# Kernel tuning notes

Hardware: AMD Instinct MI355X
Metric: run time of the kernel (lower is better)

## Reference

```python
import jax, jax.numpy as jnp
import numpy as np
from jax import lax

B, C_IN, C_OUT, KK, KS = 8, 32, 64, 4, 3
D, H, W = 32, 64, 64
PAD = 1

def setup_inputs() -> dict:
    key = jax.random.key(0)
    ks = jax.random.split(key, 12)
    s = 0.02
    return {
        "x": jax.random.normal(ks[0], (B, C_IN, D, H, W), jnp.float32),
        # K candidate conv kernels and biases
        "weight": jax.random.normal(ks[1], (KK, C_OUT, C_IN, KS, KS, KS), jnp.float32) * s,
        "cbias": jnp.zeros((KK, C_OUT), jnp.float32),
        "temperature": jnp.float32(34.0),
        # attention key path: BN(affine, eval-mode) -> GELU -> 1x1 conv (linear)
        "bn1_g": jnp.ones((C_IN,), jnp.float32),
        "bn1_b": jnp.zeros((C_IN,), jnp.float32),
        "w1": jax.random.normal(ks[2], (C_IN, C_IN), jnp.float32) * s,
        "b1": jnp.zeros((C_IN,), jnp.float32),
        "bn2_g": jnp.ones((C_IN,), jnp.float32),
        "bn2_b": jnp.zeros((C_IN,), jnp.float32),
        "w2": jax.random.normal(ks[3], (C_IN, C_IN), jnp.float32) * s,
        "b2": jnp.zeros((C_IN,), jnp.float32),
        "bn3_g": jnp.ones((C_IN,), jnp.float32),
        "bn3_b": jnp.zeros((C_IN,), jnp.float32),
        "w3": jax.random.normal(ks[4], (KK, C_IN), jnp.float32) * s,
        "b3": jnp.zeros((KK,), jnp.float32),
    }

def _attention(p, temperature, bn1_g, bn1_b, w1, b1, bn2_g, bn2_b, w2, b2, bn3_g, bn3_b, w3, b3):
    # p: [B, C] pooled features. 1x1x1 convs on 1x1x1 maps == linear layers.
    gelu = lambda t: jax.nn.gelu(t, approximate=False)  # torch nn.GELU default is erf
    a = gelu(p * bn1_g + bn1_b)          # BN (eval: rm=0, rv=1) + GELU
    a = a @ w1.T + b1
    a = gelu(a * bn2_g + bn2_b)
    a = a @ w2.T + b2
    a = a + p                            # ResidualLayer (plain add)
    a = a * bn3_g + bn3_b
    logits = a @ w3.T + b3               # [B, K]
    return jax.nn.softmax(logits / temperature, axis=1)

def reference(x, weight, cbias, temperature, bn1_g, bn1_b, w1, b1,
              bn2_g, bn2_b, w2, b2, bn3_g, bn3_b, w3, b3):
    # x: [B, C_in, D, H, W]
    p = x.mean(axis=(2, 3, 4))  # AdaptiveAvgPool3d(1)
    attn = _attention(p, temperature, bn1_g, bn1_b, w1, b1,
                      bn2_g, bn2_b, w2, b2, bn3_g, bn3_b, w3, b3)  # [B, K]
    # per-sample aggregated kernels / bias
    agg_w = jnp.einsum('bk,koidhw->boidhw', attn, weight)  # [B, O, I, k, k, k]
    agg_b = attn @ cbias                                    # [B, O]
    # grouped-conv trick (groups=B) == per-sample conv3d -> vmap over batch
    def conv1(xi, wi):
        return lax.conv_general_dilated(
            xi[None], wi, window_strides=(1, 1, 1),
            padding=[(PAD, PAD)] * 3,
            dimension_numbers=('NCDHW', 'OIDHW', 'NCDHW'))[0]
    out = jax.vmap(conv1)(x, agg_w)  # [B, O, D, H, W]
    return out + agg_b[:, :, None, None, None]
```

## Files before the change

kernel.cpp:

```cpp
#include <hip/hip_runtime.h>
#include <hip/hip_bf16.h>
#include <math.h>

#define B_   8
#define CIN  32
#define COUT 64
#define KK_  4
#define DD   32
#define HH   64
#define WW   64
#define HW   (HH*WW)
#define DHW  (DD*HH*WW)

typedef __attribute__((ext_vector_type(8)))  short bf16x8;
typedef __attribute__((ext_vector_type(16))) float f32x16;

__device__ __forceinline__ unsigned short f2bf(float f) {
    union { float f; unsigned int u; } v; v.f = f;
    return (unsigned short)((v.u + 0x7FFFu + ((v.u >> 16) & 1u)) >> 16);
}
__device__ __forceinline__ float bf2f(unsigned short s) {
    union { unsigned int u; float f; } v; v.u = ((unsigned int)s) << 16;
    return v.f;
}
__device__ __forceinline__ void gll16(const void* g, void* l) {
    __builtin_amdgcn_global_load_lds(
        (const __attribute__((address_space(1))) void*)g,
        (__attribute__((address_space(3))) void*)l, 16, 0, 0);
}

__global__ __launch_bounds__(256) void transpose_kernel(const float* __restrict__ x,
                                                        unsigned short* __restrict__ xt) {
    const int t = threadIdx.x;
    const int r = t >> 6, w = t & 63;
    const int h = (blockIdx.x << 2) + r;
    const int d = blockIdx.y, b = blockIdx.z;

    const float* xb = x + (size_t)b*CIN*DHW + (size_t)d*HW + (size_t)h*WW + w;
    unsigned int packed[CIN/2];
    #pragma unroll
    for (int c2 = 0; c2 < CIN/2; ++c2) {
        unsigned int lo = f2bf(xb[(size_t)(2*c2)   * DHW]);
        unsigned int hi = f2bf(xb[(size_t)(2*c2+1) * DHW]);
        packed[c2] = lo | (hi << 16);
    }
    char* row = (char*)xt + (size_t)((b*DD + d)*HH + h) * 4096;
    #pragma unroll
    for (int q = 0; q < 4; ++q) {
        uint4 v = make_uint4(packed[4*q], packed[4*q+1], packed[4*q+2], packed[4*q+3]);
        *(uint4*)(row + q*1024 + (((w << 4)) ^ (q << 4))) = v;
    }
}

__global__ __launch_bounds__(256) void pool2_kernel(const unsigned short* __restrict__ xt,
                                                    float* __restrict__ pblk) {
    const int t = threadIdx.x;
    const int oct = t >> 6, wi = t & 63;
    const int d = blockIdx.x, b = blockIdx.y;
    const char* base = (const char*)xt + (size_t)((b*DD + d)*HH) * 4096 + oct*1024 + wi*16;
    float acc[8];
    #pragma unroll
    for (int j = 0; j < 8; ++j) acc[j] = 0.f;
    for (int h = 0; h < HH; ++h) {
        bf16x8 v = *(const bf16x8*)(base + (size_t)h * 4096);
        #pragma unroll
        for (int j = 0; j < 8; ++j) acc[j] += bf2f((unsigned short)v[j]);
    }
    #pragma unroll
    for (int off = 32; off > 0; off >>= 1) {
        #pragma unroll
        for (int j = 0; j < 8; ++j) acc[j] += __shfl_xor(acc[j], off);
    }
    if ((t & 63) == 0) {
        #pragma unroll
        for (int j = 0; j < 8; ++j)
            pblk[(b*DD + d)*CIN + oct*8 + j] = acc[j];
    }
}

__device__ __forceinline__ float gelu_erf(float v) {
    return 0.5f * v * (1.f + erff(v * 0.70710678118654752f));
}

__global__ void attn_kernel(const float* __restrict__ pblk,
                            const float* __restrict__ temperature,
                            const float* __restrict__ bn1_g, const float* __restrict__ bn1_b,
                            const float* __restrict__ w1,    const float* __restrict__ b1,
                            const float* __restrict__ bn2_g, const float* __restrict__ bn2_b,
                            const float* __restrict__ w2,    const float* __restrict__ b2,
                            const float* __restrict__ bn3_g, const float* __restrict__ bn3_b,
                            const float* __restrict__ w3,    const float* __restrict__ b3,
                            const float* __restrict__ cbias,
                            float* __restrict__ attn_out, float* __restrict__ aggb_out) {
    __shared__ float A[B_][CIN], A2[B_][CIN];
    __shared__ float L[B_][KK_], ATT[B_][KK_];
    const int t = threadIdx.x;
    const int b = t >> 5, c = t & 31;

    float pv = 0.f;
    for (int dd = 0; dd < DD; ++dd) pv += pblk[(b*DD + dd)*CIN + c];
    pv *= (1.f / (float)DHW);

    A[b][c] = gelu_erf(pv * bn1_g[c] + bn1_b[c]);
    __syncthreads();

    float s = b1[c];
    for (int j = 0; j < CIN; ++j) s += A[b][j] * w1[c*CIN + j];
    A2[b][c] = gelu_erf(s * bn2_g[c] + bn2_b[c]);
    __syncthreads();

    float s2 = b2[c];
    for (int j = 0; j < CIN; ++j) s2 += A2[b][j] * w2[c*CIN + j];
    s2 += pv;
    s2 = s2 * bn3_g[c] + bn3_b[c];
    __syncthreads();
    A[b][c] = s2;
    __syncthreads();

    if (c < KK_) {
        float lv = b3[c];
        for (int j = 0; j < CIN; ++j) lv += A[b][j] * w3[c*CIN + j];
        L[b][c] = lv;
    }
    __syncthreads();

    const float T = temperature[0];
    if (c < KK_) {
        float m = fmaxf(fmaxf(L[b][0], L[b][1]), fmaxf(L[b][2], L[b][3]));
        float e = expf((L[b][c] - m) / T);
        float den = 0.f;
        for (int j = 0; j < KK_; ++j) den += expf((L[b][j] - m) / T);
        float av = e / den;
        ATT[b][c] = av;
        attn_out[b*KK_ + c] = av;
    }
    __syncthreads();

    for (int o = c; o < COUT; o += CIN) {
        float sb = 0.f;
        for (int k = 0; k < KK_; ++k) sb += ATT[b][k] * cbias[k*COUT + o];
        aggb_out[b*COUT + o] = sb;
    }
}

__global__ void aggw_kernel(const float* __restrict__ weight,
                            const float* __restrict__ attn,
                            unsigned short* __restrict__ wt) {
    const int idx = blockIdx.x * 256 + threadIdx.x;
    const int ci   = idx & 31;
    const int co   = (idx >> 5) & 63;
    int r          = idx >> 11;
    const int kpos = r % 27;
    const int b    = r / 27;
    float s = 0.f;
    #pragma unroll
    for (int k = 0; k < KK_; ++k)
        s += attn[b*KK_ + k] * weight[((k*COUT + co)*CIN + ci)*27 + kpos];
    wt[idx] = f2bf(s);
}

__global__ __launch_bounds__(256) void conv_mfma(const unsigned short* __restrict__ xt,
                                                 const unsigned short* __restrict__ wt,
                                                 const float* __restrict__ aggb,
                                                 float* __restrict__ out) {
    __shared__ char smem[16*4096];
    const int t = threadIdx.x;
    const int lane = t & 63, wv = t >> 6;
    const int lw = lane & 31, lh = lane >> 5;
    const int dv = wv >> 1, hv = wv & 1;
    const int h0 = blockIdx.x << 1, d0 = blockIdx.y << 1;
    const int b = blockIdx.z;

    {
        const uint4 z4 = make_uint4(0u, 0u, 0u, 0u);
        #pragma unroll
        for (int rr = 0; rr < 16; ++rr) {
            const int zd = d0 - 1 + (rr >> 2), yh = h0 - 1 + (rr & 3);
            if ((unsigned)zd >= DD || (unsigned)yh >= HH)
                *(uint4*)&smem[rr*4096 + t*16] = z4;
        }
    }
    {
        const char* xb = (const char*)xt;
        for (int rr = 0; rr < 16; ++rr) {
            const int zd = d0 - 1 + (rr >> 2), yh = h0 - 1 + (rr & 3);
            if ((unsigned)zd < DD && (unsigned)yh < HH) {
                const char* src = xb + (size_t)((b*DD + zd)*HH + yh)*4096 + wv*1024 + lane*16;
                gll16(src, &smem[rr*4096 + wv*1024]);
            }
        }
    }
    __syncthreads();

    const f32x16 fz = {};
    f32x16 acc[2][2];
    #pragma unroll
    for (int cb = 0; cb < 2; ++cb)
        #pragma unroll
        for (int fs = 0; fs < 2; ++fs)
            acc[cb][fs] = fz;

    const char* wtb = (const char*)wt + (size_t)b * 27 * 4096;
    const int a_off = lw*64 + lh*16;
    const int o0 = lh, o1 = 2 + lh;
    const bf16x8 bz = {};

    for (int kd = 0; kd < 3; ++kd) {
        for (int kh = 0; kh < 3; ++kh) {
            const int rb = (((dv + kd) << 2) + (hv + kh)) << 12;
            const char* wk0 = wtb + (size_t)((kd*3 + kh)*3) * 4096;
            #pragma unroll
            for (int kw = 0; kw < 3; ++kw) {
                const char* wk = wk0 + kw*4096;
                const bf16x8 a00 = *(const bf16x8*)(wk + a_off);
                const bf16x8 a01 = *(const bf16x8*)(wk + 32 + a_off);
                const bf16x8 a10 = *(const bf16x8*)(wk + 2048 + a_off);
                const bf16x8 a11 = *(const bf16x8*)(wk + 2048 + 32 + a_off);
                #pragma unroll
                for (int fs = 0; fs < 2; ++fs) {
                    const int wp = (fs << 5) + lw + kw - 1;
                    const bool oob = ((unsigned)wp >= (unsigned)WW);
                    const int wpc = oob ? ((wp < 0) ? 0 : (WW - 1)) : wp;
                    bf16x8 b0 = *(const bf16x8*)&smem[rb + o0*1024 + ((wpc << 4) ^ (o0 << 4))];
                    bf16x8 b1 = *(const bf16x8*)&smem[rb + o1*1024 + ((wpc << 4) ^ (o1 << 4))];
                    if (oob) { b0 = bz; b1 = bz; }
                    acc[0][fs] = __builtin_amdgcn_mfma_f32_32x32x16_bf16(a00, b0, acc[0][fs], 0, 0, 0);
                    acc[0][fs] = __builtin_amdgcn_mfma_f32_32x32x16_bf16(a01, b1, acc[0][fs], 0, 0, 0);
                    acc[1][fs] = __builtin_amdgcn_mfma_f32_32x32x16_bf16(a10, b0, acc[1][fs], 0, 0, 0);
                    acc[1][fs] = __builtin_amdgcn_mfma_f32_32x32x16_bf16(a11, b1, acc[1][fs], 0, 0, 0);
                }
            }
        }
    }

    const int d = d0 + dv, h = h0 + hv;
    float* ob = out + (size_t)b*COUT*DHW + (size_t)(d*HH + h)*WW;
    const float* ab = aggb + b*COUT;
    #pragma unroll
    for (int cb = 0; cb < 2; ++cb) {
        #pragma unroll
        for (int reg = 0; reg < 16; ++reg) {
            const int co = (cb << 5) + (reg & 3) + ((reg >> 2) << 3) + (lh << 2);
            const float bb = ab[co];
            ob[(size_t)co*DHW + lw]      = acc[cb][0][reg] + bb;
            ob[(size_t)co*DHW + 32 + lw] = acc[cb][1][reg] + bb;
        }
    }
}

extern "C" void kernel_launch(void* const* d_in, const int* in_sizes, int n_in,
                              void* d_out, int out_size, void* d_ws, size_t ws_size,
                              hipStream_t stream) {
    const float* x           = (const float*)d_in[0];
    const float* weight      = (const float*)d_in[1];
    const float* cbias       = (const float*)d_in[2];
    const float* temperature = (const float*)d_in[3];
    const float* bn1_g       = (const float*)d_in[4];
    const float* bn1_b       = (const float*)d_in[5];
    const float* w1          = (const float*)d_in[6];
    const float* b1          = (const float*)d_in[7];
    const float* bn2_g       = (const float*)d_in[8];
    const float* bn2_b       = (const float*)d_in[9];
    const float* w2          = (const float*)d_in[10];
    const float* b2          = (const float*)d_in[11];
    const float* bn3_g       = (const float*)d_in[12];
    const float* bn3_b       = (const float*)d_in[13];
    const float* w3          = (const float*)d_in[14];
    const float* b3          = (const float*)d_in[15];
    float* out = (float*)d_out;

    char* ws = (char*)d_ws;
    float*          attn = (float*)(ws + 1024);
    float*          aggb = (float*)(ws + 2048);
    float*          pblk = (float*)(ws + 16384);
    unsigned short* wt   = (unsigned short*)(ws + 65536);
    unsigned short* xt   = (unsigned short*)(ws + (1u << 20));

    transpose_kernel<<<dim3(HH/4, DD, B_), 256, 0, stream>>>(x, xt);
    pool2_kernel<<<dim3(DD, B_), 256, 0, stream>>>(xt, pblk);
    attn_kernel<<<1, 256, 0, stream>>>(pblk, temperature,
                                       bn1_g, bn1_b, w1, b1,
                                       bn2_g, bn2_b, w2, b2,
                                       bn3_g, bn3_b, w3, b3,
                                       cbias, attn, aggb);
    aggw_kernel<<<(B_*27*COUT*CIN)/256, 256, 0, stream>>>(weight, attn, wt);
    conv_mfma<<<dim3(HH/2, DD/2, B_), 256, 0, stream>>>(xt, wt, aggb, out);
}
```

Measured before the change: 215.7 us.

## Stream depth slices through an LDS ring buffer so each conv block reuses halos

Each conv block now covers 16 depth slices instead of 2. Input slices are staged into an 8-slot LDS ring, two new slices per step, so neighbouring output depths reuse the same halo planes rather than each block reloading its own. The bias is folded into the accumulator initialisation. In exchange the grid shrinks about eightfold and LDS per block doubles to 128KB, which lowers occupancy and exposes load latency behind a barrier on every step.

Result: slower. 346.8 us (+60.8%).

```diff
diff --git a/kernel.cpp b/kernel.cpp
--- a/kernel.cpp
+++ b/kernel.cpp
@@ -163,88 +163,102 @@
                                                  const unsigned short* __restrict__ wt,
                                                  const float* __restrict__ aggb,
                                                  float* __restrict__ out) {
-    __shared__ char smem[16*4096];
+    __shared__ char smem[8 * 16384];
     const int t = threadIdx.x;
     const int lane = t & 63, wv = t >> 6;
     const int lw = lane & 31, lh = lane >> 5;
-    const int dv = wv >> 1, hv = wv & 1;
-    const int h0 = blockIdx.x << 1, d0 = blockIdx.y << 1;
-    const int b = blockIdx.z;
-
-    {
-        const uint4 z4 = make_uint4(0u, 0u, 0u, 0u);
-        #pragma unroll
-        for (int rr = 0; rr < 16; ++rr) {
-            const int zd = d0 - 1 + (rr >> 2), yh = h0 - 1 + (rr & 3);
-            if ((unsigned)zd >= DD || (unsigned)yh >= HH)
-                *(uint4*)&smem[rr*4096 + t*16] = z4;
+    const int hv = wv & 1, dv = wv >> 1;
+    const int h0 = blockIdx.x << 1;
+    const int d0 = blockIdx.y << 4;
+    const int b  = blockIdx.z;
+
+    const char* xb = (const char*)xt + (size_t)(b*DD)*HH*4096;
+    const int yh_st = h0 - 1 + wv;
+    const bool yh_ok = ((unsigned)yh_st < HH);
+
+    auto stage = [&](int zd) {
+        char* ldsrow = &smem[((zd & 7) << 14) + (wv << 12)];
+        if (((unsigned)zd < DD) && yh_ok) {
+            const char* src = xb + (size_t)(zd*HH + yh_st)*4096 + lane*16;
+            #pragma unroll
+            for (int i = 0; i < 4; ++i)
+                gll16(src + i*1024, ldsrow + i*1024);
+        } else if (zd <= DD) {
+            #pragma unroll
+            for (int i = 0; i < 4; ++i)
+                *(uint4*)(ldsrow + i*1024 + lane*16) = make_uint4(0u,0u,0u,0u);
         }
-    }
-    {
-        const char* xb = (const char*)xt;
-        for (int rr = 0; rr < 16; ++rr) {
-            const int zd = d0 - 1 + (rr >> 2), yh = h0 - 1 + (rr & 3);
-            if ((unsigned)zd < DD && (unsigned)yh < HH) {
-                const char* src = xb + (size_t)((b*DD + zd)*HH + yh)*4096 + wv*1024 + lane*16;
-                gll16(src, &smem[rr*4096 + wv*1024]);
-            }
-        }
-    }
-    __syncthreads();
-
-    const f32x16 fz = {};
-    f32x16 acc[2][2];
-    #pragma unroll
-    for (int cb = 0; cb < 2; ++cb)
-        #pragma unroll
-        for (int fs = 0; fs < 2; ++fs)
-            acc[cb][fs] = fz;
+    };
 
     const char* wtb = (const char*)wt + (size_t)b * 27 * 4096;
     const int a_off = lw*64 + lh*16;
     const int o0 = lh, o1 = 2 + lh;
     const bf16x8 bz = {};
 
-    for (int kd = 0; kd < 3; ++kd) {
-        for (int kh = 0; kh < 3; ++kh) {
-            const int rb = (((dv + kd) << 2) + (hv + kh)) << 12;
-            const char* wk0 = wtb + (size_t)((kd*3 + kh)*3) * 4096;
+    f32x16 binit0, binit1;
+    #pragma unroll
+    for (int reg = 0; reg < 16; ++reg) {
+        const int cr = (reg & 3) + ((reg >> 2) << 3) + (lh << 2);
+        binit0[reg] = aggb[b*COUT + cr];
+        binit1[reg] = aggb[b*COUT + 32 + cr];
+    }
+
+    stage(d0 - 1); stage(d0); stage(d0 + 1); stage(d0 + 2);
+    __syncthreads();
+
+    const int h = h0 + hv;
+
+    for (int s = 0; s < 8; ++s) {
+        const int d = d0 + (s << 1);
+        if (s < 7) { stage(d + 3); stage(d + 4); }
+
+        const int dmy = d + dv;
+        f32x16 acc[2][2];
+        acc[0][0] = binit0; acc[0][1] = binit0;
+        acc[1][0] = binit1; acc[1][1] = binit1;
+
+        #pragma unroll
+        for (int kd = 0; kd < 3; ++kd) {
+            const int zd = dmy + kd - 1;
+            const int sb = (zd & 7) << 14;
             #pragma unroll
-            for (int kw = 0; kw < 3; ++kw) {
-                const char* wk = wk0 + kw*4096;
-                const bf16x8 a00 = *(const bf16x8*)(wk + a_off);
-                const bf16x8 a01 = *(const bf16x8*)(wk + 32 + a_off);
-                const bf16x8 a10 = *(const bf16x8*)(wk + 2048 + a_off);
-                const bf16x8 a11 = *(const bf16x8*)(wk + 2048 + 32 + a_off);
+            for (int kh = 0; kh < 3; ++kh) {
+                const int rb = sb + ((hv + kh) << 12);
+                const char* wk0 = wtb + (size_t)((kd*3 + kh)*3) * 4096;
                 #pragma unroll
-                for (int fs = 0; fs < 2; ++fs) {
-                    const int wp = (fs << 5) + lw + kw - 1;
-                    const bool oob = ((unsigned)wp >= (unsigned)WW);
-                    const int wpc = oob ? ((wp < 0) ? 0 : (WW - 1)) : wp;
-                    bf16x8 b0 = *(const bf16x8*)&smem[rb + o0*1024 + ((wpc << 4) ^ (o0 << 4))];
-                    bf16x8 b1 = *(const bf16x8*)&smem[rb + o1*1024 + ((wpc << 4) ^ (o1 << 4))];
-                    if (oob) { b0 = bz; b1 = bz; }
-                    acc[0][fs] = __builtin_amdgcn_mfma_f32_32x32x16_bf16(a00, b0, acc[0][fs], 0, 0, 0);
-                    acc[0][fs] = __builtin_amdgcn_mfma_f32_32x32x16_bf16(a01, b1, acc[0][fs], 0, 0, 0);
-                    acc[1][fs] = __builtin_amdgcn_mfma_f32_32x32x16_bf16(a10, b0, acc[1][fs], 0, 0, 0);
-                    acc[1][fs] = __builtin_amdgcn_mfma_f32_32x32x16_bf16(a11, b1, acc[1][fs], 0, 0, 0);
+                for (int kw = 0; kw < 3; ++kw) {
+                    const char* wk = wk0 + (size_t)kw * 4096;
+                    const bf16x8 a00 = *(const bf16x8*)(wk + a_off);
+                    const bf16x8 a01 = *(const bf16x8*)(wk + 32 + a_off);
+                    const bf16x8 a10 = *(const bf16x8*)(wk + 2048 + a_off);
+                    const bf16x8 a11 = *(const bf16x8*)(wk + 2048 + 32 + a_off);
+                    #pragma unroll
+                    for (int fs = 0; fs < 2; ++fs) {
+                        const int wp = (fs << 5) + lw + kw - 1;
+                        const bool oob = ((unsigned)wp >= (unsigned)WW);
+                        const int wpc = oob ? ((wp < 0) ? 0 : (WW - 1)) : wp;
+                        bf16x8 b0v = *(const bf16x8*)&smem[rb + o0*1024 + ((wpc << 4) ^ (o0 << 4))];
+                        bf16x8 b1v = *(const bf16x8*)&smem[rb + o1*1024 + ((wpc << 4) ^ (o1 << 4))];
+                        if (oob) { b0v = bz; b1v = bz; }
+                        acc[0][fs] = __builtin_amdgcn_mfma_f32_32x32x16_bf16(a00, b0v, acc[0][fs], 0, 0, 0);
+                        acc[1][fs] = __builtin_amdgcn_mfma_f32_32x32x16_bf16(a10, b0v, acc[1][fs], 0, 0, 0);
+                        acc[0][fs] = __builtin_amdgcn_mfma_f32_32x32x16_bf16(a01, b1v, acc[0][fs], 0, 0, 0);
+                        acc[1][fs] = __builtin_amdgcn_mfma_f32_32x32x16_bf16(a11, b1v, acc[1][fs], 0, 0, 0);
+                    }
                 }
             }
         }
-    }
-
-    const int d = d0 + dv, h = h0 + hv;
-    float* ob = out + (size_t)b*COUT*DHW + (size_t)(d*HH + h)*WW;
-    const float* ab = aggb + b*COUT;
-    #pragma unroll
-    for (int cb = 0; cb < 2; ++cb) {
+
+        float* ob = out + (size_t)b*COUT*DHW + (size_t)(dmy*HH + h)*WW;
         #pragma unroll
         for (int reg = 0; reg < 16; ++reg) {
-            const int co = (cb << 5) + (reg & 3) + ((reg >> 2) << 3) + (lh << 2);
-            const float bb = ab[co];
-            ob[(size_t)co*DHW + lw]      = acc[cb][0][reg] + bb;
-            ob[(size_t)co*DHW + 32 + lw] = acc[cb][1][reg] + bb;
+            const int cr = (reg & 3) + ((reg >> 2) << 3) + (lh << 2);
+            ob[(size_t)cr*DHW + lw]             = acc[0][0][reg];
+            ob[(size_t)cr*DHW + 32 + lw]        = acc[0][1][reg];
+            ob[(size_t)(32 + cr)*DHW + lw]      = acc[1][0][reg];
+            ob[(size_t)(32 + cr)*DHW + 32 + lw] = acc[1][1][reg];
         }
+        __syncthreads();
     }
 }
 
@@ -284,5 +298,5 @@
                                        bn3_g, bn3_b, w3, b3,
                                        cbias, attn, aggb);
     aggw_kernel<<<(B_*27*COUT*CIN)/256, 256, 0, stream>>>(weight, attn, wt);
-    conv_mfma<<<dim3(HH/2, DD/2, B_), 256, 0, stream>>>(xt, wt, aggb, out);
-}
+    conv_mfma<<<dim3(HH/2, DD/16, B_), 256, 0, stream>>>(xt, wt, aggb, out);
+}
```

## Enlarge conv tile to 4x4 d-h rows per block with register reuse over depth

Applied to the files above, without the earlier changes.

The conv kernel now computes a 4(d) x 4(h) x 64(w) output tile per 512-thread block instead of 2x2. Each wave keeps four depth-row accumulators, so one weight fragment load feeds several MFMAs and input rows loaded from LDS are reused across kd. Halo rows are staged in 36 LDS row buffers, with the last two h-rows loaded while earlier rows are being computed. This cuts redundant halo staging and weight reloads, but raises register pressure (8 accumulators plus 12 cached B fragments), uses a much larger LDS footprint, and launches fewer blocks.

Measured after the change: 191.3 us. 11.3% less time.

```diff
diff --git a/kernel.cpp b/kernel.cpp
--- a/kernel.cpp
+++ b/kernel.cpp
@@ -159,91 +159,113 @@
     wt[idx] = f2bf(s);
 }
 
-__global__ __launch_bounds__(256) void conv_mfma(const unsigned short* __restrict__ xt,
-                                                 const unsigned short* __restrict__ wt,
-                                                 const float* __restrict__ aggb,
-                                                 float* __restrict__ out) {
-    __shared__ char smem[16*4096];
-    const int t = threadIdx.x;
-    const int lane = t & 63, wv = t >> 6;
-    const int lw = lane & 31, lh = lane >> 5;
-    const int dv = wv >> 1, hv = wv & 1;
-    const int h0 = blockIdx.x << 1, d0 = blockIdx.y << 1;
-    const int b = blockIdx.z;
-
-    {
-        const uint4 z4 = make_uint4(0u, 0u, 0u, 0u);
-        #pragma unroll
-        for (int rr = 0; rr < 16; ++rr) {
-            const int zd = d0 - 1 + (rr >> 2), yh = h0 - 1 + (rr & 3);
-            if ((unsigned)zd >= DD || (unsigned)yh >= HH)
-                *(uint4*)&smem[rr*4096 + t*16] = z4;
+__global__ __launch_bounds__(512, 2) void conv_mfma(const unsigned short* __restrict__ xt,
+                                                    const unsigned short* __restrict__ wt,
+                                                    const float* __restrict__ aggb,
+                                                    float* __restrict__ out) {
+    __shared__ char smem[36 * 4096];
+    const int t    = threadIdx.x;
+    const int lane = t & 63;
+    const int wid  = t >> 6;
+    const int wv   = wid & 1;
+    const int hv   = wid >> 1;
+    const int lw   = lane & 31, lh = lane >> 5;
+    const int h0   = blockIdx.x << 2;
+    const int d0   = blockIdx.y << 2;
+    const int b    = blockIdx.z;
+
+    const char* xb  = (const char*)xt + (size_t)(b*DD)*HH*4096;
+    const char* wtb = (const char*)wt + (size_t)b * 27 * 4096;
+
+    auto stage_row = [&](int zo, int ho) {
+        const int zd = d0 - 1 + zo, yh = h0 - 1 + ho;
+        char* dst = smem + (size_t)((zo*6 + ho) << 12);
+        if ((unsigned)zd < DD && (unsigned)yh < HH) {
+            const char* src = xb + (size_t)(zd*HH + yh)*4096 + lane*16;
+            #pragma unroll
+            for (int q = 0; q < 4; ++q) gll16(src + (q << 10), dst + (q << 10));
+        } else {
+            #pragma unroll
+            for (int q = 0; q < 4; ++q)
+                *(uint4*)(dst + (q << 10) + lane*16) = make_uint4(0u,0u,0u,0u);
         }
-    }
-    {
-        const char* xb = (const char*)xt;
-        for (int rr = 0; rr < 16; ++rr) {
-            const int zd = d0 - 1 + (rr >> 2), yh = h0 - 1 + (rr & 3);
-            if ((unsigned)zd < DD && (unsigned)yh < HH) {
-                const char* src = xb + (size_t)((b*DD + zd)*HH + yh)*4096 + wv*1024 + lane*16;
-                gll16(src, &smem[rr*4096 + wv*1024]);
+    };
+
+    #pragma unroll
+    for (int i = 0; i < 3; ++i) {
+        const int rid = wid*3 + i;
+        stage_row(rid % 6, rid / 6);
+    }
+    __syncthreads();
+    if (wid < 6) stage_row(wid, 4);
+
+    f32x16 acc[4][2];
+    #pragma unroll
+    for (int r = 0; r < 4; ++r) {
+        acc[r][0] = (f32x16){};
+        acc[r][1] = (f32x16){};
+    }
+
+    const int a_off = lw*64 + lh*16;
+    const bf16x8 bz = {};
+    const int o0 = lh, o1 = 2 + lh;
+
+    #pragma unroll
+    for (int kh = 0; kh < 3; ++kh) {
+        if (kh == 1) {
+            __syncthreads();
+            if (wid < 6) stage_row(wid, 5);
+        }
+        if (kh == 2) __syncthreads();
+        const int ho = hv + kh;
+        #pragma unroll
+        for (int kw = 0; kw < 3; ++kw) {
+            const int wp  = (wv << 5) + lw + kw - 1;
+            const bool oob = ((unsigned)wp >= (unsigned)WW);
+            const int wpc = oob ? ((wp < 0) ? 0 : (WW - 1)) : wp;
+            const int sw0 = (o0 << 10) + ((wpc << 4) ^ (o0 << 4));
+            const int sw1 = (o1 << 10) + ((wpc << 4) ^ (o1 << 4));
+
+            bf16x8 bc[6][2];
+            #pragma unroll
+            for (int zo = 0; zo < 6; ++zo) {
+                const int rb = (zo*6 + ho) << 12;
+                bf16x8 v0 = *(const bf16x8*)&smem[rb + sw0];
+                bf16x8 v1 = *(const bf16x8*)&smem[rb + sw1];
+                bc[zo][0] = oob ? bz : v0;
+                bc[zo][1] = oob ? bz : v1;
             }
-        }
-    }
-    __syncthreads();
-
-    const f32x16 fz = {};
-    f32x16 acc[2][2];
-    #pragma unroll
-    for (int cb = 0; cb < 2; ++cb)
-        #pragma unroll
-        for (int fs = 0; fs < 2; ++fs)
-            acc[cb][fs] = fz;
-
-    const char* wtb = (const char*)wt + (size_t)b * 27 * 4096;
-    const int a_off = lw*64 + lh*16;
-    const int o0 = lh, o1 = 2 + lh;
-    const bf16x8 bz = {};
-
-    for (int kd = 0; kd < 3; ++kd) {
-        for (int kh = 0; kh < 3; ++kh) {
-            const int rb = (((dv + kd) << 2) + (hv + kh)) << 12;
-            const char* wk0 = wtb + (size_t)((kd*3 + kh)*3) * 4096;
-            #pragma unroll
-            for (int kw = 0; kw < 3; ++kw) {
-                const char* wk = wk0 + kw*4096;
+            #pragma unroll
+            for (int kd = 0; kd < 3; ++kd) {
+                const char* wk = wtb + (size_t)(((kd*3 + kh)*3 + kw) << 12);
                 const bf16x8 a00 = *(const bf16x8*)(wk + a_off);
                 const bf16x8 a01 = *(const bf16x8*)(wk + 32 + a_off);
                 const bf16x8 a10 = *(const bf16x8*)(wk + 2048 + a_off);
                 const bf16x8 a11 = *(const bf16x8*)(wk + 2048 + 32 + a_off);
                 #pragma unroll
-                for (int fs = 0; fs < 2; ++fs) {
-                    const int wp = (fs << 5) + lw + kw - 1;
-                    const bool oob = ((unsigned)wp >= (unsigned)WW);
-                    const int wpc = oob ? ((wp < 0) ? 0 : (WW - 1)) : wp;
-                    bf16x8 b0 = *(const bf16x8*)&smem[rb + o0*1024 + ((wpc << 4) ^ (o0 << 4))];
-                    bf16x8 b1 = *(const bf16x8*)&smem[rb + o1*1024 + ((wpc << 4) ^ (o1 << 4))];
-                    if (oob) { b0 = bz; b1 = bz; }
-                    acc[0][fs] = __builtin_amdgcn_mfma_f32_32x32x16_bf16(a00, b0, acc[0][fs], 0, 0, 0);
-                    acc[0][fs] = __builtin_amdgcn_mfma_f32_32x32x16_bf16(a01, b1, acc[0][fs], 0, 0, 0);
-                    acc[1][fs] = __builtin_amdgcn_mfma_f32_32x32x16_bf16(a10, b0, acc[1][fs], 0, 0, 0);
-                    acc[1][fs] = __builtin_amdgcn_mfma_f32_32x32x16_bf16(a11, b1, acc[1][fs], 0, 0, 0);
+                for (int r = 0; r < 4; ++r) {
+                    const int zo = r + kd;
+                    acc[r][0] = __builtin_amdgcn_mfma_f32_32x32x16_bf16(a00, bc[zo][0], acc[r][0], 0, 0, 0);
+                    acc[r][0] = __builtin_amdgcn_mfma_f32_32x32x16_bf16(a01, bc[zo][1], acc[r][0], 0, 0, 0);
+                    acc[r][1] = __builtin_amdgcn_mfma_f32_32x32x16_bf16(a10, bc[zo][0], acc[r][1], 0, 0, 0);
+                    acc[r][1] = __builtin_amdgcn_mfma_f32_32x32x16_bf16(a11, bc[zo][1], acc[r][1], 0, 0, 0);
                 }
             }
         }
     }
 
-    const int d = d0 + dv, h = h0 + hv;
-    float* ob = out + (size_t)b*COUT*DHW + (size_t)(d*HH + h)*WW;
     const float* ab = aggb + b*COUT;
+    const int sp0 = (h0 + hv)*WW + (wv << 5) + lw;
     #pragma unroll
     for (int cb = 0; cb < 2; ++cb) {
         #pragma unroll
         for (int reg = 0; reg < 16; ++reg) {
             const int co = (cb << 5) + (reg & 3) + ((reg >> 2) << 3) + (lh << 2);
             const float bb = ab[co];
-            ob[(size_t)co*DHW + lw]      = acc[cb][0][reg] + bb;
-            ob[(size_t)co*DHW + 32 + lw] = acc[cb][1][reg] + bb;
+            float* oc = out + ((size_t)(b*COUT + co))*DHW + sp0;
+            #pragma unroll
+            for (int r = 0; r < 4; ++r)
+                oc[(size_t)(d0 + r)*HW] = acc[r][cb][reg] + bb;
         }
     }
 }
@@ -284,5 +306,5 @@
                                        bn3_g, bn3_b, w3, b3,
                                        cbias, attn, aggb);
     aggw_kernel<<<(B_*27*COUT*CIN)/256, 256, 0, stream>>>(weight, attn, wt);
-    conv_mfma<<<dim3(HH/2, DD/2, B_), 256, 0, stream>>>(xt, wt, aggb, out);
-}
+    conv_mfma<<<dim3(HH/4, DD/4, B_), 512, 0, stream>>>(xt, wt, aggb, out);
+}
```
